# Performance work log

Measured on AMD Instinct MI355X. Metric: run time of the kernel, lower is better.

Reference implementation:

```python
import jax, jax.numpy as jnp
import numpy as np

N = 100000
E = 1600000
F_IN = 512
HEADS = 8
C1 = 8          # per-head channels layer 1
C2 = 16         # num_classes, layer 2 (heads=1)
NEG_SLOPE = 0.2


def gat_conv(x, W, att_src, att_dst, bias, edge_index, heads, ch):
    """PyG-style GATConv (eval mode, add_self_loops=True, concat).
    x: [N, Fin], W: [Fin, heads*ch], att_*: [heads, ch], bias: [heads*ch]."""
    n = x.shape[0]
    loop = jnp.arange(n, dtype=edge_index.dtype)
    src = jnp.concatenate([edge_index[0], loop])   # [E+N]
    dst = jnp.concatenate([edge_index[1], loop])

    h = (x @ W).reshape(n, heads, ch)                       # [N, H, C]
    a_src = jnp.einsum('nhc,hc->nh', h, att_src)            # [N, H]
    a_dst = jnp.einsum('nhc,hc->nh', h, att_dst)

    e = a_src[src] + a_dst[dst]                             # [E+N, H]
    e = jax.nn.leaky_relu(e, NEG_SLOPE)
    # segment softmax over destination nodes
    m = jax.ops.segment_max(e, dst, num_segments=n)         # [N, H]
    ex = jnp.exp(e - m[dst])
    denom = jax.ops.segment_sum(ex, dst, num_segments=n)    # [N, H]
    alpha = ex / (denom[dst] + 1e-16)                       # [E+N, H]

    msg = h[src] * alpha[..., None]                         # [E+N, H, C]
    out = jax.ops.segment_sum(msg, dst, num_segments=n)     # [N, H, C]
    return out.reshape(n, heads * ch) + bias


def setup_inputs() -> dict:
    key = jax.random.key(0)
    ks = jax.random.split(key, 10)
    glorot = lambda k, shape: jax.random.normal(k, shape, jnp.float32) * np.sqrt(2.0 / (shape[0] + shape[-1]))
    return {
        'x': jax.random.normal(ks[0], (N, F_IN), jnp.float32),
        'edge_index': jax.random.randint(ks[1], (2, E), 0, N, jnp.int64),
        'W1': glorot(ks[2], (F_IN, HEADS * C1)),
        'att_src1': glorot(ks[3], (HEADS, C1)),
        'att_dst1': glorot(ks[4], (HEADS, C1)),
        'b1': jnp.zeros((HEADS * C1,), jnp.float32),
        'W2': glorot(ks[5], (HEADS * C1, C2)),
        'att_src2': glorot(ks[6], (1, C2)),
        'att_dst2': glorot(ks[7], (1, C2)),
        'b2': jnp.zeros((C2,), jnp.float32),
    }


def reference(x, edge_index, W1, att_src1, att_dst1, b1, W2, att_src2, att_dst2, b2):
    # eval mode: all F.dropout / internal attention dropout are identity
    h = gat_conv(x, W1, att_src1, att_dst1, b1, edge_index, HEADS, C1)   # [N, 64]
    h = jax.nn.elu(h)
    h = gat_conv(h, W2, att_src2, att_dst2, b2, edge_index, 1, C2)       # [N, C2]
    return jax.nn.log_softmax(h, axis=1)
```

## Files before the change

kernel.cpp:

```cpp
#include <hip/hip_runtime.h>
#include <hip/hip_bf16.h>

#define NEG_SLOPE 0.2f

typedef __attribute__((ext_vector_type(8))) short  bf16x8;
typedef __attribute__((ext_vector_type(8))) unsigned short u16x8;
typedef __attribute__((ext_vector_type(4))) unsigned short u16x4;
typedef __attribute__((ext_vector_type(4))) float  f32x4;

static __device__ __forceinline__ ushort f2bf(float f) {
    union { float f; unsigned int u; } c; c.f = f;
    unsigned int r = c.u + 0x7fffu + ((c.u >> 16) & 1u);
    return (ushort)(r >> 16);
}
static __device__ __forceinline__ float bf2f(ushort u) {
    union { unsigned int u; float f; } c; c.u = ((unsigned int)u) << 16;
    return c.f;
}

__global__ __launch_bounds__(256) void phase1_k(
    const float* __restrict__ W, ushort* __restrict__ W1T,
    const int* __restrict__ ei, int* __restrict__ cnt, int* __restrict__ slot, int E)
{
    if (blockIdx.x < 128) {
        int idx = blockIdx.x * 256 + threadIdx.x;
        int c = idx >> 9, k = idx & 511;
        W1T[idx] = f2bf(W[k * 64 + c]);
    } else {
        int t = (blockIdx.x - 128) * 256 + threadIdx.x;
        if (t < E) slot[t] = atomicAdd(&cnt[ei[E + t]], 1);
    }
}

#define SCAN_B 256
#define SCAN_T 256

__global__ __launch_bounds__(SCAN_T) void scan_a(const int* __restrict__ cnt, int* __restrict__ bsum, int n)
{
    __shared__ int sh[SCAN_T];
    const int tid = threadIdx.x;
    const int per = (n + SCAN_B * SCAN_T - 1) / (SCAN_B * SCAN_T);
    const int lo = (blockIdx.x * SCAN_T + tid) * per;
    const int hi = min(n, lo + per);
    int s = 0;
    for (int i = lo; i < hi; ++i) s += cnt[i];
    sh[tid] = s;
    __syncthreads();
    #pragma unroll
    for (int o = SCAN_T / 2; o; o >>= 1) {
        if (tid < o) sh[tid] += sh[tid + o];
        __syncthreads();
    }
    if (tid == 0) bsum[blockIdx.x] = sh[0];
}

__global__ __launch_bounds__(SCAN_T) void scan_b(
    const int* __restrict__ cnt, const int* __restrict__ bsum,
    int* __restrict__ rowptr, int n, int E)
{
    __shared__ int sb[SCAN_B];
    __shared__ int sh[SCAN_T];
    const int tid = threadIdx.x;
    sb[tid] = bsum[tid];
    __syncthreads();
    #pragma unroll
    for (int o = 1; o < SCAN_B; o <<= 1) {
        int v = (tid >= o) ? sb[tid - o] : 0;
        __syncthreads();
        sb[tid] += v;
        __syncthreads();
    }
    const int boff = (blockIdx.x == 0) ? 0 : sb[blockIdx.x - 1];

    const int per = (n + SCAN_B * SCAN_T - 1) / (SCAN_B * SCAN_T);
    const int lo = (blockIdx.x * SCAN_T + tid) * per;
    const int hi = min(n, lo + per);
    int s = 0;
    for (int i = lo; i < hi; ++i) s += cnt[i];
    sh[tid] = s;
    __syncthreads();
    #pragma unroll
    for (int o = 1; o < SCAN_T; o <<= 1) {
        int v = (tid >= o) ? sh[tid - o] : 0;
        __syncthreads();
        sh[tid] += v;
        __syncthreads();
    }
    int excl = boff + ((tid == 0) ? 0 : sh[tid - 1]);
    for (int i = lo; i < hi; ++i) { rowptr[i] = excl; excl += cnt[i]; }
    if (blockIdx.x == 0 && tid == 0) rowptr[n] = E;
}

__global__ __launch_bounds__(512, 4) void phase4_k(
    const int* __restrict__ ei, const int* __restrict__ rowptr,
    const int* __restrict__ slot, int* __restrict__ ssrc, int E, int Gs,
    const float* __restrict__ x, const ushort* __restrict__ W1T,
    const float* __restrict__ att_src, const float* __restrict__ att_dst,
    ushort* __restrict__ h1b, float* __restrict__ asrc, float* __restrict__ adst, int n)
{
    __shared__ ushort Bs[64][520];

    if ((int)blockIdx.x < Gs) {
        int t = blockIdx.x * 512 + threadIdx.x;
        if (t < E) {
            int d = ei[E + t];
            ssrc[rowptr[d] + slot[t]] = ei[t];
        }
        return;
    }

    const int t    = threadIdx.x;
    const int lane = t & 63;
    const int wv   = t >> 6;
    const int rb   = (blockIdx.x - Gs) * 128;
    const int m    = lane & 15;
    const int kg   = lane >> 4;

    #pragma unroll
    for (int i = 0; i < 8; ++i) {
        int chunk = t + i * 512;
        int c  = chunk >> 6;
        int ko = (chunk & 63) * 8;
        *(u16x8*)&Bs[c][ko] = *(const u16x8*)(W1T + c * 512 + ko);
    }

    const int arow  = rb + wv * 16 + m;
    const int arowc = min(arow, n - 1);
    const float* xp = x + (size_t)arowc * 512 + kg * 8;

    f32x4 acc[4] = {};
    __syncthreads();

    float4 plo[4], phi[4];
    #pragma unroll
    for (int i = 0; i < 4; ++i) {
        plo[i] = *(const float4*)(xp + i * 32);
        phi[i] = *(const float4*)(xp + i * 32 + 4);
    }
    #pragma unroll
    for (int k32 = 0; k32 < 16; ++k32) {
        float4 lo = plo[k32 & 3], hi = phi[k32 & 3];
        if (k32 + 4 < 16) {
            plo[k32 & 3] = *(const float4*)(xp + (k32 + 4) * 32);
            phi[k32 & 3] = *(const float4*)(xp + (k32 + 4) * 32 + 4);
        }
        u16x8 a;
        a[0] = f2bf(lo.x); a[1] = f2bf(lo.y); a[2] = f2bf(lo.z); a[3] = f2bf(lo.w);
        a[4] = f2bf(hi.x); a[5] = f2bf(hi.y); a[6] = f2bf(hi.z); a[7] = f2bf(hi.w);
        bf16x8 af = *(bf16x8*)&a;
        #pragma unroll
        for (int t4 = 0; t4 < 4; ++t4) {
            bf16x8 bfr = *(const bf16x8*)&Bs[t4 * 16 + m][k32 * 32 + kg * 8];
            acc[t4] = __builtin_amdgcn_mfma_f32_16x16x32_bf16(af, bfr, acc[t4], 0, 0, 0);
        }
    }

    #pragma unroll
    for (int t4 = 0; t4 < 4; ++t4) {
        const float as_w = att_src[t4 * 16 + m];
        const float ad_w = att_dst[t4 * 16 + m];
        #pragma unroll
        for (int i = 0; i < 4; ++i) {
            int gr = rb + wv * 16 + kg * 4 + i;
            float v = acc[t4][i];
            float ps = v * as_w, pd = v * ad_w;
            ps += __shfl_xor(ps, 1); pd += __shfl_xor(pd, 1);
            ps += __shfl_xor(ps, 2); pd += __shfl_xor(pd, 2);
            ps += __shfl_xor(ps, 4); pd += __shfl_xor(pd, 4);
            if (gr < n) {
                h1b[(size_t)gr * 64 + t4 * 16 + m] = f2bf(v);
                if ((m & 7) == 0) {
                    int h = t4 * 2 + (m >> 3);
                    asrc[gr * 8 + h] = ps;
                    adst[gr * 8 + h] = pd;
                }
            }
        }
    }
}

__global__ __launch_bounds__(256) void agg1_k(
    const int* __restrict__ rowptr, const int* __restrict__ ssrc,
    const float* __restrict__ asrc1, const float* __restrict__ adst1,
    const ushort* __restrict__ h1b, const float* __restrict__ b1,
    const float* __restrict__ W2, const float* __restrict__ att_src2, const float* __restrict__ att_dst2,
    ushort* __restrict__ h2b, float* __restrict__ asrc2, float* __restrict__ adst2, int n)
{
    __shared__ float Ws2[64 * 17];
    __shared__ float sv[4][64];
    const int t = threadIdx.x;
    #pragma unroll
    for (int k = 0; k < 4; ++k) {
        int idx = t + k * 256;
        Ws2[(idx >> 4) * 17 + (idx & 15)] = W2[idx];
    }
    __syncthreads();

    const int wv = t >> 6;
    const int j  = t & 63;
    const int g  = j >> 3;
    const int h  = j & 7;
    const int node = blockIdx.x * 4 + wv;
    const bool active = node < n;

    if (active) {
        const int d = node;
        const int start = rowptr[d], end = rowptr[d + 1];
        const float adsth = adst1[d * 8 + h];
        float acc0[8] = {}, acc1[8] = {};
        float dsum0 = 0.f, dsum1 = 0.f;
        for (int base = start - 1; base < end; base += 16) {
            int i0 = base + g;
            int i1 = i0 + 8;
            if (i0 < end) {
                int s = (i0 < start) ? d : ssrc[i0];
                float e = asrc1[s * 8 + h] + adsth;
                e = e > 0.f ? e : NEG_SLOPE * e;
                float ex = __expf(e);
                dsum0 += ex;
                u16x8 hv = *(const u16x8*)(h1b + (size_t)s * 64 + h * 8);
                #pragma unroll
                for (int c = 0; c < 8; ++c) acc0[c] += ex * bf2f(hv[c]);
            }
            if (i1 < end) {
                int s = ssrc[i1];
                float e = asrc1[s * 8 + h] + adsth;
                e = e > 0.f ? e : NEG_SLOPE * e;
                float ex = __expf(e);
                dsum1 += ex;
                u16x8 hv = *(const u16x8*)(h1b + (size_t)s * 64 + h * 8);
                #pragma unroll
                for (int c = 0; c < 8; ++c) acc1[c] += ex * bf2f(hv[c]);
            }
        }
        float dsum = dsum0 + dsum1;
        float acc[8];
        #pragma unroll
        for (int c = 0; c < 8; ++c) acc[c] = acc0[c] + acc1[c];
        #pragma unroll
        for (int o = 8; o < 64; o <<= 1) {
            dsum += __shfl_xor(dsum, o);
            #pragma unroll
            for (int c = 0; c < 8; ++c) acc[c] += __shfl_xor(acc[c], o);
        }
        if (g == 0) {
            float den = dsum + 1e-16f;
            #pragma unroll
            for (int c = 0; c < 8; ++c) {
                float v = acc[c] / den + b1[h * 8 + c];
                v = v > 0.f ? v : (__expf(v) - 1.f);
                sv[wv][h * 8 + c] = v;
            }
        }
    }
    __syncthreads();

    if (active) {
        const int c = j & 15, q = j >> 4;
        float p = 0.f;
        #pragma unroll
        for (int r = 0; r < 16; ++r)
            p += sv[wv][q * 16 + r] * Ws2[(q * 16 + r) * 17 + c];
        p += __shfl_xor(p, 16);
        p += __shfl_xor(p, 32);
        if (j < 16) h2b[(size_t)node * 16 + j] = f2bf(p);
        float as2 = p * att_src2[c];
        float ad2 = p * att_dst2[c];
        #pragma unroll
        for (int o = 1; o < 16; o <<= 1) { as2 += __shfl_xor(as2, o, 16); ad2 += __shfl_xor(ad2, o, 16); }
        if (j == 0) { asrc2[node] = as2; adst2[node] = ad2; }
    }
}

__global__ __launch_bounds__(256) void agg2_k(
    const int* __restrict__ rowptr, const int* __restrict__ ssrc,
    const float* __restrict__ asrc2, const float* __restrict__ adst2,
    const ushort* __restrict__ h2b, const float* __restrict__ b2,
    float* __restrict__ out, int n)
{
    const int t = threadIdx.x;
    const int node = blockIdx.x * 4 + (t >> 6);
    if (node >= n) return;
    const int j = t & 63;
    const int g = j >> 2;
    const int q = j & 3;
    const int d = node;
    const int start = rowptr[d], end = rowptr[d + 1];
    const float adst_d = adst2[d];

    float acc0[4] = {}, acc1[4] = {};
    float dsum0 = 0.f, dsum1 = 0.f;
    for (int base = start - 1; base < end; base += 32) {
        int i0 = base + g;
        int i1 = i0 + 16;
        if (i0 < end) {
            int s = (i0 < start) ? d : ssrc[i0];
            float e = asrc2[s] + adst_d;
            e = e > 0.f ? e : NEG_SLOPE * e;
            float ex = __expf(e);
            dsum0 += ex;
            u16x4 hv = *(const u16x4*)(h2b + (size_t)s * 16 + q * 4);
            #pragma unroll
            for (int c = 0; c < 4; ++c) acc0[c] += ex * bf2f(hv[c]);
        }
        if (i1 < end) {
            int s = ssrc[i1];
            float e = asrc2[s] + adst_d;
            e = e > 0.f ? e : NEG_SLOPE * e;
            float ex = __expf(e);
            dsum1 += ex;
            u16x4 hv = *(const u16x4*)(h2b + (size_t)s * 16 + q * 4);
            #pragma unroll
            for (int c = 0; c < 4; ++c) acc1[c] += ex * bf2f(hv[c]);
        }
    }
    float dsum = dsum0 + dsum1;
    float acc[4];
    #pragma unroll
    for (int c = 0; c < 4; ++c) acc[c] = acc0[c] + acc1[c];
    #pragma unroll
    for (int o = 4; o < 64; o <<= 1) {
        dsum += __shfl_xor(dsum, o);
        #pragma unroll
        for (int c = 0; c < 4; ++c) acc[c] += __shfl_xor(acc[c], o);
    }

    const float den = dsum + 1e-16f;
    float v[4];
    float m = -1e30f;
    #pragma unroll
    for (int c = 0; c < 4; ++c) {
        v[c] = acc[c] / den + b2[q * 4 + c];
        m = fmaxf(m, v[c]);
    }
    m = fmaxf(m, __shfl_xor(m, 1));
    m = fmaxf(m, __shfl_xor(m, 2));
    float s2 = 0.f;
    #pragma unroll
    for (int c = 0; c < 4; ++c) s2 += __expf(v[c] - m);
    s2 += __shfl_xor(s2, 1);
    s2 += __shfl_xor(s2, 2);
    const float lse = m + logf(s2);
    if (j < 4) {
        float4 o4 = make_float4(v[0] - lse, v[1] - lse, v[2] - lse, v[3] - lse);
        *(float4*)(out + (size_t)d * 16 + q * 4) = o4;
    }
}

static inline size_t align_up(size_t v, size_t a) { return (v + a - 1) & ~(a - 1); }

extern "C" void kernel_launch(void* const* d_in, const int* in_sizes, int n_in,
                              void* d_out, int out_size, void* d_ws, size_t ws_size,
                              hipStream_t stream) {
    const float* x        = (const float*)d_in[0];
    const int*   ei       = (const int*)d_in[1];
    const float* W1       = (const float*)d_in[2];
    const float* att_src1 = (const float*)d_in[3];
    const float* att_dst1 = (const float*)d_in[4];
    const float* b1       = (const float*)d_in[5];
    const float* W2       = (const float*)d_in[6];
    const float* att_src2 = (const float*)d_in[7];
    const float* att_dst2 = (const float*)d_in[8];
    const float* b2       = (const float*)d_in[9];
    float* out = (float*)d_out;

    const int n = in_sizes[0] / 512;
    const int E = in_sizes[1] / 2;

    char* base = (char*)d_ws;
    size_t off = 0;
    ushort* h1b   = (ushort*)(base + off); off = align_up(off + (size_t)128 * n, 64);
    ushort* h2b   = (ushort*)(base + off); off = align_up(off + (size_t)32 * n, 64);
    float*  asrc1 = (float*) (base + off); off = align_up(off + (size_t)32 * n, 64);
    float*  adst1 = (float*) (base + off); off = align_up(off + (size_t)32 * n, 64);
    float*  asrc2 = (float*) (base + off); off = align_up(off + (size_t)4 * n, 64);
    float*  adst2 = (float*) (base + off); off = align_up(off + (size_t)4 * n, 64);
    ushort* W1T   = (ushort*)(base + off); off = align_up(off + (size_t)65536, 64);
    int*    rowptr= (int*)   (base + off); off = align_up(off + (size_t)4 * (n + 1), 64);
    int*    cnt   = (int*)   (base + off); off = align_up(off + (size_t)4 * n, 64);
    int*    bsum  = (int*)   (base + off); off = align_up(off + (size_t)1024, 64);
    int*    slot  = (int*)   (base + off); off = align_up(off + (size_t)4 * E, 64);
    int*    ssrc  = (int*)   (base + off);

    hipMemsetAsync(cnt, 0, (size_t)4 * n, stream);

    phase1_k<<<128 + (E + 255) / 256, 256, 0, stream>>>(W1, W1T, ei, cnt, slot, E);

    scan_a<<<SCAN_B, SCAN_T, 0, stream>>>(cnt, bsum, n);
    scan_b<<<SCAN_B, SCAN_T, 0, stream>>>(cnt, bsum, rowptr, n, E);

    const int Gs = (E + 511) / 512;
    const int Gg = (n + 127) / 128;
    phase4_k<<<Gs + Gg, 512, 0, stream>>>(ei, rowptr, slot, ssrc, E, Gs,
                                          x, W1T, att_src1, att_dst1, h1b, asrc1, adst1, n);

    agg1_k<<<(n + 3) / 4, 256, 0, stream>>>(rowptr, ssrc, asrc1, adst1, h1b, b1,
                                            W2, att_src2, att_dst2, h2b, asrc2, adst2, n);

    agg2_k<<<(n + 3) / 4, 256, 0, stream>>>(rowptr, ssrc, asrc2, adst2, h2b, b2, out, n);
}
```

Baseline: 268.5 us.

## Interleave scatter and GEMM blocks, halve W1 LDS tile for higher occupancy

The fused phase4 kernel now spreads its GEMM blocks evenly among the edge-scatter blocks instead of putting them all at the end. The W1 tile in shared memory is halved by loading the K dimension in two 256-wide passes, and the launch-bounds occupancy hint rises from 4 to 8 blocks. The x prefetch depth drops from four stages to two. The aim is to overlap the memory-bound scatter with the MFMA work and fit more blocks per CU, at the cost of an extra barrier pair and less prefetch per GEMM block.

```diff
diff --git a/kernel.cpp b/kernel.cpp
--- a/kernel.cpp
+++ b/kernel.cpp
@@ -91,17 +91,21 @@
     if (blockIdx.x == 0 && tid == 0) rowptr[n] = E;
 }
 
-__global__ __launch_bounds__(512, 4) void phase4_k(
+__global__ __launch_bounds__(512, 8) void phase4_k(
     const int* __restrict__ ei, const int* __restrict__ rowptr,
-    const int* __restrict__ slot, int* __restrict__ ssrc, int E, int Gs,
+    const int* __restrict__ slot, int* __restrict__ ssrc, int E, int Gs, int Gg, int per,
     const float* __restrict__ x, const ushort* __restrict__ W1T,
     const float* __restrict__ att_src, const float* __restrict__ att_dst,
     ushort* __restrict__ h1b, float* __restrict__ asrc, float* __restrict__ adst, int n)
 {
-    __shared__ ushort Bs[64][520];
-
-    if ((int)blockIdx.x < Gs) {
-        int t = blockIdx.x * 512 + threadIdx.x;
+    __shared__ ushort Bs[64][264];
+
+    const int bid = blockIdx.x;
+    const bool is_gemm = (bid % per == 0) && (bid / per < Gg);
+
+    if (!is_gemm) {
+        int sid = bid - min(bid / per + 1, Gg);
+        int t = sid * 512 + threadIdx.x;
         if (t < E) {
             int d = ei[E + t];
             ssrc[rowptr[d] + slot[t]] = ei[t];
@@ -112,47 +116,51 @@
     const int t    = threadIdx.x;
     const int lane = t & 63;
     const int wv   = t >> 6;
-    const int rb   = (blockIdx.x - Gs) * 128;
+    const int rb   = (bid / per) * 128;
     const int m    = lane & 15;
     const int kg   = lane >> 4;
-
-    #pragma unroll
-    for (int i = 0; i < 8; ++i) {
-        int chunk = t + i * 512;
-        int c  = chunk >> 6;
-        int ko = (chunk & 63) * 8;
-        *(u16x8*)&Bs[c][ko] = *(const u16x8*)(W1T + c * 512 + ko);
-    }
 
     const int arow  = rb + wv * 16 + m;
     const int arowc = min(arow, n - 1);
     const float* xp = x + (size_t)arowc * 512 + kg * 8;
 
     f32x4 acc[4] = {};
-    __syncthreads();
-
-    float4 plo[4], phi[4];
-    #pragma unroll
-    for (int i = 0; i < 4; ++i) {
-        plo[i] = *(const float4*)(xp + i * 32);
-        phi[i] = *(const float4*)(xp + i * 32 + 4);
-    }
-    #pragma unroll
-    for (int k32 = 0; k32 < 16; ++k32) {
-        float4 lo = plo[k32 & 3], hi = phi[k32 & 3];
-        if (k32 + 4 < 16) {
-            plo[k32 & 3] = *(const float4*)(xp + (k32 + 4) * 32);
-            phi[k32 & 3] = *(const float4*)(xp + (k32 + 4) * 32 + 4);
-        }
-        u16x8 a;
-        a[0] = f2bf(lo.x); a[1] = f2bf(lo.y); a[2] = f2bf(lo.z); a[3] = f2bf(lo.w);
-        a[4] = f2bf(hi.x); a[5] = f2bf(hi.y); a[6] = f2bf(hi.z); a[7] = f2bf(hi.w);
-        bf16x8 af = *(bf16x8*)&a;
-        #pragma unroll
-        for (int t4 = 0; t4 < 4; ++t4) {
-            bf16x8 bfr = *(const bf16x8*)&Bs[t4 * 16 + m][k32 * 32 + kg * 8];
-            acc[t4] = __builtin_amdgcn_mfma_f32_16x16x32_bf16(af, bfr, acc[t4], 0, 0, 0);
-        }
+
+    #pragma unroll
+    for (int h = 0; h < 2; ++h) {
+        #pragma unroll
+        for (int i = 0; i < 4; ++i) {
+            int chunk = t + i * 512;
+            int c  = chunk >> 5;
+            int ko = (chunk & 31) * 8;
+            *(u16x8*)&Bs[c][ko] = *(const u16x8*)(W1T + c * 512 + h * 256 + ko);
+        }
+        __syncthreads();
+
+        const float* xh = xp + h * 256;
+        float4 lo0 = *(const float4*)(xh);
+        float4 hi0 = *(const float4*)(xh + 4);
+        float4 lo1 = *(const float4*)(xh + 32);
+        float4 hi1 = *(const float4*)(xh + 36);
+        #pragma unroll
+        for (int k32 = 0; k32 < 8; ++k32) {
+            float4 nlo = {}, nhi = {};
+            if (k32 < 6) {
+                nlo = *(const float4*)(xh + (k32 + 2) * 32);
+                nhi = *(const float4*)(xh + (k32 + 2) * 32 + 4);
+            }
+            u16x8 a;
+            a[0] = f2bf(lo0.x); a[1] = f2bf(lo0.y); a[2] = f2bf(lo0.z); a[3] = f2bf(lo0.w);
+            a[4] = f2bf(hi0.x); a[5] = f2bf(hi0.y); a[6] = f2bf(hi0.z); a[7] = f2bf(hi0.w);
+            bf16x8 af = *(bf16x8*)&a;
+            #pragma unroll
+            for (int t4 = 0; t4 < 4; ++t4) {
+                bf16x8 bfr = *(const bf16x8*)&Bs[t4 * 16 + m][k32 * 32 + kg * 8];
+                acc[t4] = __builtin_amdgcn_mfma_f32_16x16x32_bf16(af, bfr, acc[t4], 0, 0, 0);
+            }
+            lo0 = lo1; hi0 = hi1; lo1 = nlo; hi1 = nhi;
+        }
+        __syncthreads();
     }
 
     #pragma unroll
@@ -391,8 +399,10 @@
 
     const int Gs = (E + 511) / 512;
     const int Gg = (n + 127) / 128;
-    phase4_k<<<Gs + Gg, 512, 0, stream>>>(ei, rowptr, slot, ssrc, E, Gs,
-                                          x, W1T, att_src1, att_dst1, h1b, asrc1, adst1, n);
+    const int total = Gs + Gg;
+    const int per = total / Gg;
+    phase4_k<<<total, 512, 0, stream>>>(ei, rowptr, slot, ssrc, E, Gs, Gg, per,
+                                        x, W1T, att_src1, att_dst1, h1b, asrc1, adst1, n);
 
     agg1_k<<<(n + 3) / 4, 256, 0, stream>>>(rowptr, ssrc, asrc1, adst1, h1b, b1,
                                             W2, att_src2, att_dst2, h2b, asrc2, adst2, n);
```

New measurement: 334.2 us. 1.24x slower.

## Split fused scatter/GEMM kernel and halve GEMM LDS tile via K-split staging

Applied to the files above, without the earlier changes.

Splits the combined CSR-scatter and layer-1 GEMM kernel into two separate launches, so the GEMM runs after the scatter instead of sharing one grid with it. The GEMM now stages W1T into shared memory in two K-halves of 256, which halves the LDS footprint per block and should allow more resident blocks. The cost is an extra kernel launch, an extra barrier per half, and losing the overlap between the scatter and the GEMM.

```diff
diff --git a/kernel.cpp b/kernel.cpp
--- a/kernel.cpp
+++ b/kernel.cpp
@@ -91,67 +91,70 @@
     if (blockIdx.x == 0 && tid == 0) rowptr[n] = E;
 }
 
-__global__ __launch_bounds__(512, 4) void phase4_k(
+__global__ __launch_bounds__(256) void scatter_k(
     const int* __restrict__ ei, const int* __restrict__ rowptr,
-    const int* __restrict__ slot, int* __restrict__ ssrc, int E, int Gs,
+    const int* __restrict__ slot, int* __restrict__ ssrc, int E)
+{
+    int t = blockIdx.x * blockDim.x + threadIdx.x;
+    if (t >= E) return;
+    int d = ei[E + t];
+    ssrc[rowptr[d] + slot[t]] = ei[t];
+}
+
+__global__ __launch_bounds__(512, 4) void gemm1_mfma(
     const float* __restrict__ x, const ushort* __restrict__ W1T,
     const float* __restrict__ att_src, const float* __restrict__ att_dst,
     ushort* __restrict__ h1b, float* __restrict__ asrc, float* __restrict__ adst, int n)
 {
-    __shared__ ushort Bs[64][520];
-
-    if ((int)blockIdx.x < Gs) {
-        int t = blockIdx.x * 512 + threadIdx.x;
-        if (t < E) {
-            int d = ei[E + t];
-            ssrc[rowptr[d] + slot[t]] = ei[t];
-        }
-        return;
-    }
-
+    __shared__ ushort Bs[64][264];
     const int t    = threadIdx.x;
     const int lane = t & 63;
     const int wv   = t >> 6;
-    const int rb   = (blockIdx.x - Gs) * 128;
+    const int rb   = blockIdx.x * 128;
     const int m    = lane & 15;
     const int kg   = lane >> 4;
-
-    #pragma unroll
-    for (int i = 0; i < 8; ++i) {
-        int chunk = t + i * 512;
-        int c  = chunk >> 6;
-        int ko = (chunk & 63) * 8;
-        *(u16x8*)&Bs[c][ko] = *(const u16x8*)(W1T + c * 512 + ko);
-    }
 
     const int arow  = rb + wv * 16 + m;
     const int arowc = min(arow, n - 1);
     const float* xp = x + (size_t)arowc * 512 + kg * 8;
 
     f32x4 acc[4] = {};
-    __syncthreads();
-
-    float4 plo[4], phi[4];
-    #pragma unroll
-    for (int i = 0; i < 4; ++i) {
-        plo[i] = *(const float4*)(xp + i * 32);
-        phi[i] = *(const float4*)(xp + i * 32 + 4);
-    }
-    #pragma unroll
-    for (int k32 = 0; k32 < 16; ++k32) {
-        float4 lo = plo[k32 & 3], hi = phi[k32 & 3];
-        if (k32 + 4 < 16) {
-            plo[k32 & 3] = *(const float4*)(xp + (k32 + 4) * 32);
-            phi[k32 & 3] = *(const float4*)(xp + (k32 + 4) * 32 + 4);
-        }
-        u16x8 a;
-        a[0] = f2bf(lo.x); a[1] = f2bf(lo.y); a[2] = f2bf(lo.z); a[3] = f2bf(lo.w);
-        a[4] = f2bf(hi.x); a[5] = f2bf(hi.y); a[6] = f2bf(hi.z); a[7] = f2bf(hi.w);
-        bf16x8 af = *(bf16x8*)&a;
-        #pragma unroll
-        for (int t4 = 0; t4 < 4; ++t4) {
-            bf16x8 bfr = *(const bf16x8*)&Bs[t4 * 16 + m][k32 * 32 + kg * 8];
-            acc[t4] = __builtin_amdgcn_mfma_f32_16x16x32_bf16(af, bfr, acc[t4], 0, 0, 0);
+
+    #pragma unroll
+    for (int h = 0; h < 2; ++h) {
+        if (h) __syncthreads();
+        #pragma unroll
+        for (int i = 0; i < 4; ++i) {
+            int chunk = t + i * 512;
+            int c  = chunk >> 5;
+            int ko = (chunk & 31) * 8;
+            *(u16x8*)&Bs[c][ko] = *(const u16x8*)(W1T + c * 512 + h * 256 + ko);
+        }
+        __syncthreads();
+
+        const float* xh = xp + h * 256;
+        float4 plo[4], phi[4];
+        #pragma unroll
+        for (int i = 0; i < 4; ++i) {
+            plo[i] = *(const float4*)(xh + i * 32);
+            phi[i] = *(const float4*)(xh + i * 32 + 4);
+        }
+        #pragma unroll
+        for (int k32 = 0; k32 < 8; ++k32) {
+            float4 lo = plo[k32 & 3], hi = phi[k32 & 3];
+            if (k32 < 4) {
+                plo[k32 & 3] = *(const float4*)(xh + (k32 + 4) * 32);
+                phi[k32 & 3] = *(const float4*)(xh + (k32 + 4) * 32 + 4);
+            }
+            u16x8 a;
+            a[0] = f2bf(lo.x); a[1] = f2bf(lo.y); a[2] = f2bf(lo.z); a[3] = f2bf(lo.w);
+            a[4] = f2bf(hi.x); a[5] = f2bf(hi.y); a[6] = f2bf(hi.z); a[7] = f2bf(hi.w);
+            bf16x8 af = *(bf16x8*)&a;
+            #pragma unroll
+            for (int t4 = 0; t4 < 4; ++t4) {
+                bf16x8 bfr = *(const bf16x8*)&Bs[t4 * 16 + m][k32 * 32 + kg * 8];
+                acc[t4] = __builtin_amdgcn_mfma_f32_16x16x32_bf16(af, bfr, acc[t4], 0, 0, 0);
+            }
         }
     }
 
@@ -389,10 +392,9 @@
     scan_a<<<SCAN_B, SCAN_T, 0, stream>>>(cnt, bsum, n);
     scan_b<<<SCAN_B, SCAN_T, 0, stream>>>(cnt, bsum, rowptr, n, E);
 
-    const int Gs = (E + 511) / 512;
-    const int Gg = (n + 127) / 128;
-    phase4_k<<<Gs + Gg, 512, 0, stream>>>(ei, rowptr, slot, ssrc, E, Gs,
-                                          x, W1T, att_src1, att_dst1, h1b, asrc1, adst1, n);
+    scatter_k<<<(E + 255) / 256, 256, 0, stream>>>(ei, rowptr, slot, ssrc, E);
+
+    gemm1_mfma<<<(n + 127) / 128, 512, 0, stream>>>(x, W1T, att_src1, att_dst1, h1b, asrc1, adst1, n);
 
     agg1_k<<<(n + 3) / 4, 256, 0, stream>>>(rowptr, ssrc, asrc1, adst1, h1b, b1,
                                             W2, att_src2, att_dst2, h2b, asrc2, adst2, n);
```

Measured after the change: 276.8 us. 3.1% more time.
